# Kernel optimization log

Hardware: AMD Instinct MI355X
Metric: run time of the kernel (lower is better)

The kernel has to match this reference:

```python
import jax, jax.numpy as jnp
import numpy as np

N = 50000      # nodes
E = 1000000    # edges per edge set
D_IN = 2000
D_H = 20
EPS = 1e-5     # BatchNorm eps
SLOPE = 0.01   # leaky_relu negative slope


def setup_inputs() -> dict:
    key = jax.random.key(0)
    ks = jax.random.split(key, 32)
    w = lambda i, shape: jax.random.normal(ks[i], shape, jnp.float32) * 0.05
    inp = {}
    inp["features"] = jax.random.normal(ks[0], (N, D_IN), jnp.float32)
    inp["same_index"] = jax.random.randint(ks[1], (2, 16), 0, N, jnp.int32)
    inp["diff_index"] = jax.random.randint(ks[2], (2, 16), 0, N, jnp.int32)
    inp["edge_index"] = jax.random.randint(ks[3], (2, E), 0, N, jnp.int32)
    inp["same_index2"] = jax.random.randint(ks[4], (2, E), 0, N, jnp.int32)
    inp["diff_index2"] = jax.random.randint(ks[5], (2, E), 0, N, jnp.int32)
    # TransformerConv weights packed as [q,k,v,skip] along axis 0
    inp["c1_W0"] = w(6, (4, D_IN, D_H)); inp["c1_b0"] = w(7, (4, D_H))
    inp["c2_W0"] = w(8, (4, D_IN, D_H)); inp["c2_b0"] = w(9, (4, D_H))
    inp["c1_W"] = w(10, (4, 4, 2 * D_H, D_H)); inp["c1_b"] = w(11, (4, 4, D_H))
    inp["c2_W"] = w(12, (4, 4, 2 * D_H, D_H)); inp["c2_b"] = w(13, (4, 4, D_H))
    inp["c3_W"] = w(14, (5, 4, 2 * D_H, D_H)); inp["c3_b"] = w(15, (5, 4, D_H))  # conv13..17
    inp["bn1_g"] = jnp.ones((5, D_H), jnp.float32); inp["bn1_b"] = w(16, (5, D_H))
    inp["bn2_g"] = jnp.ones((5, D_H), jnp.float32); inp["bn2_b"] = w(17, (5, D_H))
    inp["bn3_g"] = jnp.ones((5, D_H), jnp.float32); inp["bn3_b"] = w(18, (5, D_H))
    inp["fc_W"] = w(19, (5 * D_H, 2)); inp["fc_b"] = w(20, (2,))
    return inp


def _tconv(x, ei, W, b):
    """PyG TransformerConv, heads=1, root_weight=True, concat=True.
    W: [4, Din, 20] = (Wq, Wk, Wv, Wskip); b: [4, 20]."""
    src, dst = ei[0], ei[1]
    q = x @ W[0] + b[0]          # [N,20]
    k = x @ W[1] + b[1]
    v = x @ W[2] + b[2]
    logits = jnp.sum(q[dst] * k[src], axis=-1) / jnp.sqrt(jnp.float32(D_H))  # [E]
    m = jax.ops.segment_max(logits, dst, num_segments=N)
    m = jnp.where(jnp.isfinite(m), m, 0.0)
    e = jnp.exp(logits - m[dst])
    denom = jax.ops.segment_sum(e, dst, num_segments=N)
    alpha = e / jnp.maximum(denom[dst], 1e-16)
    agg = jax.ops.segment_sum(alpha[:, None] * v[src], dst, num_segments=N)  # [N,20]
    return agg + x @ W[3] + b[3]


def _bn(x, g, b):
    mu = jnp.mean(x, axis=0)
    var = jnp.mean(jnp.square(x - mu), axis=0)
    return g * (x - mu) * jax.lax.rsqrt(var + EPS) + b


def _lrelu(x):
    return jnp.where(x >= 0, x, SLOPE * x)


def reference(features, same_index, diff_index, edge_index, same_index2, diff_index2,
              c1_W0, c1_b0, c2_W0, c2_b0, c1_W, c1_b, c2_W, c2_b, c3_W, c3_b,
              bn1_g, bn1_b, bn2_g, bn2_b, bn3_g, bn3_b, fc_W, fc_b):
    # dropout is identity (eval mode)
    x = features
    x1 = _lrelu(_bn(_tconv(x, same_index2, c1_W0, c1_b0), bn1_g[0], bn1_b[0]))
    x2 = _lrelu(_bn(_tconv(x, diff_index2, c2_W0, c2_b0), bn2_g[0], bn2_b[0]))
    h = jnp.concatenate([x1, x2], axis=-1)
    h = _lrelu(_bn(_tconv(h, edge_index, c3_W[0], c3_b[0]), bn3_g[0], bn3_b[0]))
    fc = h
    for l in range(4):
        x3 = jnp.concatenate([x1, x2], axis=-1)
        x4 = jnp.concatenate([x2, x1], axis=-1)
        x1 = _lrelu(_bn(_tconv(x3, same_index2, c1_W[l], c1_b[l]), bn1_g[l + 1], bn1_b[l + 1]))
        x2 = _lrelu(_bn(_tconv(x4, diff_index2, c2_W[l], c2_b[l]), bn2_g[l + 1], bn2_b[l + 1]))
        h = jnp.concatenate([x1, x2], axis=-1)
        h = _lrelu(_bn(_tconv(h, edge_index, c3_W[l + 1], c3_b[l + 1]), bn3_g[l + 1], bn3_b[l + 1]))
        fc = jnp.concatenate([fc, h], axis=-1)
    return fc @ fc_W + fc_b  # [N, 2]
```

## Files before the change

kernel.cpp:

```cpp
#include <hip/hip_runtime.h>
#include <stddef.h>

#define NN 50000
#define NE 1000000
#define SLOT 64
#define RSQRT20 0.22360679774997896f

typedef __attribute__((ext_vector_type(8))) short s16x8;
typedef __attribute__((ext_vector_type(4))) float f32x4;

__device__ __forceinline__ unsigned short f2bf(float x) {
  union { float f; unsigned int u; } cv; cv.f = x;
  unsigned int u = cv.u + 0x7fffu + ((cv.u >> 16) & 1u);
  return (unsigned short)(u >> 16);
}
__device__ __forceinline__ float bf2f(unsigned short h) {
  union { unsigned int u; float f; } cv; cv.u = ((unsigned int)h) << 16;
  return cv.f;
}

__global__ __launch_bounds__(256) void k_zero(int* __restrict__ p, int n) {
  int i = blockIdx.x * 256 + threadIdx.x;
  if (i < n) p[i] = 0;
}

__global__ __launch_bounds__(256) void k_fill(
    const int* __restrict__ s0, const int* __restrict__ d0,
    const int* __restrict__ s1, const int* __restrict__ d1,
    const int* __restrict__ s2, const int* __restrict__ d2,
    int* __restrict__ c0, int* __restrict__ c1, int* __restrict__ c2,
    int* __restrict__ r0, int* __restrict__ r1, int* __restrict__ r2) {
  int e = blockIdx.x * 256 + threadIdx.x;
  if (e >= NE) return;
  const int* s; const int* d; int* c; int* r;
  if (blockIdx.y == 0)      { s = s0; d = d0; c = c0; r = r0; }
  else if (blockIdx.y == 1) { s = s1; d = d1; c = c1; r = r1; }
  else                      { s = s2; d = d2; c = c2; r = r2; }
  int dn = d[e];
  int pos = atomicAdd(&c[dn], 1);
  if (pos < SLOT) r[dn * SLOT + pos] = s[e];
}

__global__ __launch_bounds__(256) void k_packB(
    const float* __restrict__ W1, const float* __restrict__ W2,
    unsigned short* __restrict__ BtH, unsigned short* __restrict__ BtL) {
  int gid = blockIdx.x * 256 + threadIdx.x;
  if (gid >= 160 * 2000) return;
  int col = gid / 2000, k = gid - col * 2000;
  int s = col >= 80; int cc = col - s * 80; int jm = cc / 20, f = cc - jm * 20;
  const float* Wp = s ? W2 : W1;
  float w = Wp[(jm * 2000 + k) * 20 + f];
  unsigned short h = f2bf(w);
  BtH[(size_t)col * 2000 + k] = h;
  BtL[(size_t)col * 2000 + k] = f2bf(w - bf2f(h));
}

__global__ __launch_bounds__(256) void k_mm0(
    const float* __restrict__ X,
    const unsigned short* __restrict__ BtHg, const unsigned short* __restrict__ BtLg,
    const float* __restrict__ B1, const float* __restrict__ B2,
    float* __restrict__ proj, float* __restrict__ stats) {
  __shared__ __attribute__((aligned(16))) char AsH[64 * 128];
  __shared__ __attribute__((aligned(16))) char AsL[64 * 128];
  __shared__ __attribute__((aligned(16))) char BsH[160 * 128];
  __shared__ __attribute__((aligned(16))) char BsL[160 * 128];
  int tid = threadIdx.x;
  if (blockIdx.x == 0 && tid < 120) stats[tid] = 0.f;
  int rowbase = blockIdx.x * 64;
  int l = tid & 63, w = tid >> 6;
  int l15 = l & 15, lq = l >> 4;

  f32x4 acc[10];
  #pragma unroll
  for (int n = 0; n < 10; ++n) acc[n] = (f32x4){0.f, 0.f, 0.f, 0.f};

  float4 aReg[4]; float4 bRegH[5]; float4 bRegL[5];
  auto issue = [&](int tt) {
    int kt = tt * 64;
    #pragma unroll
    for (int i = 0; i < 4; ++i) {
      int idx = tid + i * 256;
      int rowL = idx >> 4, q4 = idx & 15;
      int gr = rowbase + rowL;
      int kk = kt + q4 * 4;
      float4 v = make_float4(0.f, 0.f, 0.f, 0.f);
      if (gr < NN && kk + 4 <= 2000)
        v = *(const float4*)(X + (size_t)gr * 2000 + kk);
      aReg[i] = v;
    }
    #pragma unroll
    for (int i = 0; i < 5; ++i) {
      int idx = tid + i * 256;
      int col = idx >> 3, ck = idx & 7;
      int kk = kt + ck * 8;
      float4 vh = make_float4(0.f, 0.f, 0.f, 0.f);
      float4 vl = vh;
      if (kk + 8 <= 2000) {
        vh = *(const float4*)((const float*)(BtHg + (size_t)col * 2000 + kk));
        vl = *(const float4*)((const float*)(BtLg + (size_t)col * 2000 + kk));
      }
      bRegH[i] = vh; bRegL[i] = vl;
    }
  };

  issue(0);
  for (int t = 0; t < 32; ++t) {
    __syncthreads();
    #pragma unroll
    for (int i = 0; i < 4; ++i) {
      int idx = tid + i * 256;
      int rowL = idx >> 4, q4 = idx & 15;
      ushort4 hh, hl;
      {
        float v0 = aReg[i].x, v1 = aReg[i].y, v2 = aReg[i].z, v3 = aReg[i].w;
        hh.x = f2bf(v0); hl.x = f2bf(v0 - bf2f(hh.x));
        hh.y = f2bf(v1); hl.y = f2bf(v1 - bf2f(hh.y));
        hh.z = f2bf(v2); hl.z = f2bf(v2 - bf2f(hh.z));
        hh.w = f2bf(v3); hl.w = f2bf(v3 - bf2f(hh.w));
      }
      unsigned int byte = (unsigned)rowL * 128u +
          (((unsigned)(q4 * 8)) ^ ((unsigned)((rowL & 7) << 4)));
      *(ushort4*)(AsH + byte) = hh;
      *(ushort4*)(AsL + byte) = hl;
    }
    #pragma unroll
    for (int i = 0; i < 5; ++i) {
      int idx = tid + i * 256;
      int col = idx >> 3, ck = idx & 7;
      unsigned int byte = (unsigned)col * 128u +
          (((unsigned)(ck * 16)) ^ ((unsigned)((col & 7) << 4)));
      *(float4*)(BsH + byte) = bRegH[i];
      *(float4*)(BsL + byte) = bRegL[i];
    }
    __syncthreads();
    if (t < 31) issue(t + 1);
    #pragma unroll
    for (int ks = 0; ks < 2; ++ks) {
      unsigned int rowL = (unsigned)(w * 16 + l15);
      unsigned int ab = rowL * 128u +
          (((unsigned)(ks * 64 + 16 * lq)) ^ ((rowL & 7u) << 4));
      s16x8 afh = *(const s16x8*)(AsH + ab);
      s16x8 afl = *(const s16x8*)(AsL + ab);
      #pragma unroll
      for (int n = 0; n < 10; ++n) {
        unsigned int colL = (unsigned)(n * 16 + l15);
        unsigned int bb = colL * 128u +
            (((unsigned)(ks * 64 + 16 * lq)) ^ ((colL & 7u) << 4));
        s16x8 bfh = *(const s16x8*)(BsH + bb);
        s16x8 bfl = *(const s16x8*)(BsL + bb);
        acc[n] = __builtin_amdgcn_mfma_f32_16x16x32_bf16(afh, bfh, acc[n], 0, 0, 0);
        acc[n] = __builtin_amdgcn_mfma_f32_16x16x32_bf16(afh, bfl, acc[n], 0, 0, 0);
        acc[n] = __builtin_amdgcn_mfma_f32_16x16x32_bf16(afl, bfh, acc[n], 0, 0, 0);
      }
    }
  }

  #pragma unroll
  for (int n = 0; n < 10; ++n) {
    int col = n * 16 + l15;
    int sb = col / 20, f = col - sb * 20;
    float bias = (col < 80) ? B1[col] : B2[col - 80];
    float* ob = proj + (size_t)sb * 1000000;
    #pragma unroll
    for (int r = 0; r < 4; ++r) {
      int row = rowbase + w * 16 + 4 * lq + r;
      if (row < NN) ob[(size_t)row * 20 + f] = acc[n][r] + bias;
    }
  }
}

#define WSTR 812
__global__ __launch_bounds__(256) void k_proj(
    const float* __restrict__ x1, const float* __restrict__ x2,
    const float* __restrict__ W0, const float* __restrict__ B0, int mode0, int slot0,
    const float* __restrict__ W1, const float* __restrict__ B1, int mode1, int slot1,
    const float* __restrict__ W2, const float* __restrict__ B2, int mode2, int slot2,
    int nconv, float* __restrict__ proj, float* __restrict__ stats) {
  __shared__ float wl[12 * WSTR];
  int tid = threadIdx.x;
  if (blockIdx.x == 0 && tid < 120) stats[tid] = 0.f;
  for (int idx = tid; idx < nconv * 3200; idx += 256) {
    int cm = idx / 800, r = idx - cm * 800;
    int t = cm >> 2;
    const float* Wp = (t == 0) ? W0 : (t == 1 ? W1 : W2);
    wl[cm * WSTR + r] = Wp[(cm & 3) * 800 + r];
  }
  __syncthreads();
  int g = tid / 12, cm = tid - g * 12, t = cm >> 2, jm = cm & 3;
  if (g >= 21 || t >= nconv) return;
  int n0 = blockIdx.x * 84 + g * 4;
  if (n0 >= NN) return;
  const float* Bp = (t == 0) ? B0 : (t == 1 ? B1 : B2);
  int mode = (t == 0) ? mode0 : (t == 1 ? mode1 : mode2);
  int slot = (t == 0) ? slot0 : (t == 1 ? slot1 : slot2);
  const float* A  = mode ? x2 : x1;
  const float* Bx = mode ? x1 : x2;
  int nvalid = min(4, NN - n0);
  float4 acc[4][5];
  #pragma unroll
  for (int m = 0; m < 4; ++m)
    #pragma unroll
    for (int f4 = 0; f4 < 5; ++f4)
      acc[m][f4] = make_float4(Bp[jm*20 + f4*4], Bp[jm*20 + f4*4+1],
                               Bp[jm*20 + f4*4+2], Bp[jm*20 + f4*4+3]);
  const float* wbase = &wl[cm * WSTR];
  #pragma unroll 1
  for (int half = 0; half < 2; ++half) {
    const float* src = half ? Bx : A;
    for (int i = 0; i < 20; ++i) {
      float xv[4];
      #pragma unroll
      for (int m = 0; m < 4; ++m)
        xv[m] = (m < nvalid) ? src[(size_t)(n0 + m) * 20 + i] : 0.f;
      #pragma unroll
      for (int f4 = 0; f4 < 5; ++f4) {
        float4 w = *(const float4*)&wbase[(half * 20 + i) * 20 + f4 * 4];
        #pragma unroll
        for (int m = 0; m < 4; ++m) {
          acc[m][f4].x += xv[m] * w.x; acc[m][f4].y += xv[m] * w.y;
          acc[m][f4].z += xv[m] * w.z; acc[m][f4].w += xv[m] * w.w;
        }
      }
    }
  }
  float* ob = proj + (size_t)(slot + jm) * 1000000;
  #pragma unroll
  for (int m = 0; m < 4; ++m) {
    if (m < nvalid) {
      float* p = ob + (size_t)(n0 + m) * 20;
      #pragma unroll
      for (int f4 = 0; f4 < 5; ++f4) *(float4*)&p[f4*4] = acc[m][f4];
    }
  }
}

__global__ __launch_bounds__(256) void k_edge_w(
    const int* __restrict__ cnt, const int* __restrict__ csr,
    const float* __restrict__ q, const float* __restrict__ k,
    float* __restrict__ wsl) {
  int gid = blockIdx.x * 256 + threadIdx.x;
  if (gid >= NN * SLOT) return;
  int n = gid >> 6, j = gid & 63;
  int deg = min(cnt[n], SLOT);
  if (j >= deg) return;
  int s = csr[gid];
  const float* qr = q + (size_t)n * 20;
  const float* kr = k + (size_t)s * 20;
  float dot = 0.f;
  #pragma unroll
  for (int f4 = 0; f4 < 5; ++f4) {
    float4 a = *(const float4*)&qr[f4*4];
    float4 b = *(const float4*)&kr[f4*4];
    dot += a.x*b.x + a.y*b.y + a.z*b.z + a.w*b.w;
  }
  wsl[gid] = __expf(dot * RSQRT20);
}

__global__ __launch_bounds__(256) void k_edge_agg(
    const int* __restrict__ cnt, const int* __restrict__ csr,
    const float* __restrict__ wsl, const float* __restrict__ v,
    const float* __restrict__ skip, float* __restrict__ pre) {
  int gid = blockIdx.x * 256 + threadIdx.x;
  if (gid >= NN * 20) return;
  int n = gid / 20, f = gid - n * 20;
  int deg = min(cnt[n], SLOT);
  const int* cs = csr + n * SLOT;
  const float* ws = wsl + n * SLOT;
  float accd = 0.f, acca = 0.f;
  for (int j = 0; j < deg; ++j) {
    float w = ws[j];
    int s = cs[j];
    acca += w * v[(size_t)s * 20 + f];
    accd += w;
  }
  pre[gid] = acca / fmaxf(accd, 1e-16f) + skip[gid];
}

__global__ __launch_bounds__(320) void k_bnstats(
    const float* __restrict__ p0, const float* __restrict__ p1,
    const float* __restrict__ p2, float* __restrict__ stats) {
  const float* p = (blockIdx.y == 0) ? p0 : (blockIdx.y == 1 ? p1 : p2);
  __shared__ float ls[40];
  int tid = threadIdx.x;
  if (tid < 40) ls[tid] = 0.f;
  __syncthreads();
  int f = tid % 20;
  int c = blockIdx.x * 16 + tid / 20;
  float s = 0.f, sq = 0.f;
  for (int r = c; r < NN; r += 1024) {
    float v = p[r * 20 + f];
    s += v; sq += v * v;
  }
  atomicAdd(&ls[f], s);
  atomicAdd(&ls[20 + f], sq);
  __syncthreads();
  if (tid < 40) atomicAdd(&stats[blockIdx.y * 40 + tid], ls[tid]);
}

__global__ __launch_bounds__(256) void k_bnapply(int nconv,
    const float* __restrict__ pA, const float* __restrict__ gA, const float* __restrict__ bA,
    float* __restrict__ dA, int stA, int ofA,
    const float* __restrict__ pB, const float* __restrict__ gB, const float* __restrict__ bB,
    float* __restrict__ dB, int stB, int ofB,
    const float* __restrict__ pC, const float* __restrict__ gC, const float* __restrict__ bC,
    float* __restrict__ dC, int stC, int ofC,
    const float* __restrict__ stats) {
  int gid = blockIdx.x * 256 + threadIdx.x;
  if (gid >= NN * 20) return;
  int n = gid / 20, f = gid - n * 20;
  for (int c = 0; c < nconv; ++c) {
    const float* p = (c == 0) ? pA : (c == 1 ? pB : pC);
    const float* g = (c == 0) ? gA : (c == 1 ? gB : gC);
    const float* b = (c == 0) ? bA : (c == 1 ? bB : bC);
    float* d = (c == 0) ? dA : (c == 1 ? dB : dC);
    int st = (c == 0) ? stA : (c == 1 ? stB : stC);
    int of = (c == 0) ? ofA : (c == 1 ? ofB : ofC);
    float s1 = stats[c * 40 + f], s2 = stats[c * 40 + 20 + f];
    float mean = s1 * (1.0f / NN);
    float var  = fmaf(-mean, mean, s2 * (1.0f / NN));
    float inv  = rsqrtf(var + 1e-5f);
    float val  = (p[gid] - mean) * inv * g[f] + b[f];
    val = (val >= 0.f) ? val : 0.01f * val;
    d[(size_t)n * st + of + f] = val;
  }
}

__global__ __launch_bounds__(256) void k_fc(
    const float* __restrict__ fc, const float* __restrict__ W,
    const float* __restrict__ b, float* __restrict__ out) {
  int n = blockIdx.x * 256 + threadIdx.x;
  if (n >= NN) return;
  const float* row = fc + (size_t)n * 100;
  float a0 = b[0], a1 = b[1];
  for (int j = 0; j < 100; ++j) {
    float x = row[j];
    a0 += x * W[j * 2];
    a1 += x * W[j * 2 + 1];
  }
  out[n * 2]     = a0;
  out[n * 2 + 1] = a1;
}

extern "C" void kernel_launch(void* const* d_in, const int* in_sizes, int n_in,
                              void* d_out, int out_size, void* d_ws, size_t ws_size,
                              hipStream_t stream) {
  (void)in_sizes; (void)n_in; (void)out_size; (void)ws_size;
  const float* features = (const float*)d_in[0];
  const int* edge_index = (const int*)d_in[3];
  const int* same2      = (const int*)d_in[4];
  const int* diff2      = (const int*)d_in[5];
  const float* c1_W0 = (const float*)d_in[6];
  const float* c1_b0 = (const float*)d_in[7];
  const float* c2_W0 = (const float*)d_in[8];
  const float* c2_b0 = (const float*)d_in[9];
  const float* c1_W  = (const float*)d_in[10];
  const float* c1_b  = (const float*)d_in[11];
  const float* c2_W  = (const float*)d_in[12];
  const float* c2_b  = (const float*)d_in[13];
  const float* c3_W  = (const float*)d_in[14];
  const float* c3_b  = (const float*)d_in[15];
  const float* bn1_g = (const float*)d_in[16];
  const float* bn1_b = (const float*)d_in[17];
  const float* bn2_g = (const float*)d_in[18];
  const float* bn2_b = (const float*)d_in[19];
  const float* bn3_g = (const float*)d_in[20];
  const float* bn3_b = (const float*)d_in[21];
  const float* fc_W  = (const float*)d_in[22];
  const float* fc_b  = (const float*)d_in[23];
  float* out = (float*)d_out;

  char* wsb = (char*)d_ws;
  size_t off = 0;
  auto alloc = [&](size_t bytes) -> void* {
    void* p = wsb + off;
    off += (bytes + 255) & ~(size_t)255;
    return p;
  };
  int*   cntall = (int*)  alloc((size_t)3 * NN * 4);
  int*   csrall = (int*)  alloc((size_t)3 * NN * SLOT * 4);
  float* wslall = (float*)alloc((size_t)3 * NN * SLOT * 4);
  float* proj   = (float*)alloc((size_t)12 * 1000000 * 4);
  float* preA   = (float*)alloc((size_t)1000000 * 4);
  float* preB   = (float*)alloc((size_t)1000000 * 4);
  float* preC   = (float*)alloc((size_t)1000000 * 4);
  float* x1     = (float*)alloc((size_t)1000000 * 4);
  float* x2     = (float*)alloc((size_t)1000000 * 4);
  float* fcbuf  = (float*)alloc((size_t)5000000 * 4);
  float* stats  = (float*)alloc(120 * 4);
  int* cnt0 = cntall;           int* cnt1 = cntall + NN;      int* cnt2 = cntall + 2 * NN;
  int* csr0 = csrall;           int* csr1 = csrall + NN*SLOT; int* csr2 = csrall + 2*NN*SLOT;
  float* wsl0 = wslall;         float* wsl1 = wslall + NN*SLOT; float* wsl2 = wslall + 2*NN*SLOT;
  unsigned short* BtH = (unsigned short*)(proj + (size_t)8 * 1000000);
  unsigned short* BtL = BtH + (size_t)160 * 2000;

  const dim3 B256(256);
  const int gE   = (NE + 255) / 256;
  const int gNF  = (NN * 20 + 255) / 256;
  const int gSL  = (NN * SLOT) / 256;
  const int gMM  = (NN + 63) / 64;
  const int gPR  = (NN + 83) / 84;
  const int gFC  = (NN + 255) / 256;

  k_zero<<<dim3((3 * NN + 255) / 256), B256, 0, stream>>>(cntall, 3 * NN);
  k_fill<<<dim3(gE, 3), B256, 0, stream>>>(
      same2, same2 + NE, diff2, diff2 + NE, edge_index, edge_index + NE,
      cnt0, cnt1, cnt2, csr0, csr1, csr2);

  k_packB<<<dim3((160 * 2000 + 255) / 256), B256, 0, stream>>>(c1_W0, c2_W0, BtH, BtL);
  k_mm0<<<dim3(gMM), B256, 0, stream>>>(features, BtH, BtL, c1_b0, c2_b0, proj, stats);
  k_edge_w<<<dim3(gSL), B256, 0, stream>>>(cnt0, csr0, proj + 0ull,       proj + 1000000ull, wsl0);
  k_edge_w<<<dim3(gSL), B256, 0, stream>>>(cnt1, csr1, proj + 4000000ull, proj + 5000000ull, wsl1);
  k_edge_agg<<<dim3(gNF), B256, 0, stream>>>(cnt0, csr0, wsl0, proj + 2000000ull, proj + 3000000ull, preA);
  k_edge_agg<<<dim3(gNF), B256, 0, stream>>>(cnt1, csr1, wsl1, proj + 6000000ull, proj + 7000000ull, preB);
  k_bnstats<<<dim3(64, 2), dim3(320), 0, stream>>>(preA, preB, preB, stats);
  k_bnapply<<<dim3(gNF), B256, 0, stream>>>(2,
      preA, bn1_g, bn1_b, x1, 20, 0,
      preB, bn2_g, bn2_b, x2, 20, 0,
      preB, bn2_g, bn2_b, x2, 20, 0, stats);

  for (int i = 0; i < 4; ++i) {
    k_proj<<<dim3(gPR), B256, 0, stream>>>(x1, x2,
        c1_W + (size_t)i * 3200, c1_b + (size_t)i * 80, 0, 0,
        c2_W + (size_t)i * 3200, c2_b + (size_t)i * 80, 1, 4,
        c3_W + (size_t)i * 3200, c3_b + (size_t)i * 80, 0, 8,
        3, proj, stats);
    k_edge_w<<<dim3(gSL), B256, 0, stream>>>(cnt0, csr0, proj + 0ull,       proj + 1000000ull, wsl0);
    k_edge_w<<<dim3(gSL), B256, 0, stream>>>(cnt1, csr1, proj + 4000000ull, proj + 5000000ull, wsl1);
    k_edge_w<<<dim3(gSL), B256, 0, stream>>>(cnt2, csr2, proj + 8000000ull, proj + 9000000ull, wsl2);
    k_edge_agg<<<dim3(gNF), B256, 0, stream>>>(cnt0, csr0, wsl0, proj + 2000000ull,  proj + 3000000ull,  preA);
    k_edge_agg<<<dim3(gNF), B256, 0, stream>>>(cnt1, csr1, wsl1, proj + 6000000ull,  proj + 7000000ull,  preB);
    k_edge_agg<<<dim3(gNF), B256, 0, stream>>>(cnt2, csr2, wsl2, proj + 10000000ull, proj + 11000000ull, preC);
    k_bnstats<<<dim3(64, 3), dim3(320), 0, stream>>>(preA, preB, preC, stats);
    k_bnapply<<<dim3(gNF), B256, 0, stream>>>(3,
        preA, bn1_g + (i + 1) * 20, bn1_b + (i + 1) * 20, x1, 20, 0,
        preB, bn2_g + (i + 1) * 20, bn2_b + (i + 1) * 20, x2, 20, 0,
        preC, bn3_g + i * 20,       bn3_b + i * 20,       fcbuf, 100, i * 20, stats);
  }

  k_proj<<<dim3(gPR), B256, 0, stream>>>(x1, x2,
      c3_W + 4 * 3200, c3_b + 4 * 80, 0, 8,
      c3_W + 4 * 3200, c3_b + 4 * 80, 0, 0,
      c3_W + 4 * 3200, c3_b + 4 * 80, 0, 0,
      1, proj, stats);
  k_edge_w<<<dim3(gSL), B256, 0, stream>>>(cnt2, csr2, proj + 8000000ull, proj + 9000000ull, wsl2);
  k_edge_agg<<<dim3(gNF), B256, 0, stream>>>(cnt2, csr2, wsl2, proj + 10000000ull, proj + 11000000ull, preC);
  k_bnstats<<<dim3(64, 1), dim3(320), 0, stream>>>(preC, preC, preC, stats);
  k_bnapply<<<dim3(gNF), B256, 0, stream>>>(1,
      preC, bn3_g + 80, bn3_b + 80, fcbuf, 100, 80,
      preC, bn3_g + 80, bn3_b + 80, fcbuf, 100, 80,
      preC, bn3_g + 80, bn3_b + 80, fcbuf, 100, 80, stats);

  k_fc<<<dim3(gFC), B256, 0, stream>>>(fcbuf, fc_W, fc_b, out);
}
```

Baseline: 2.105 ms.

## Fuse edge attention weight and aggregation kernels, store CSR indices as u16

The separate per-edge weight kernel and per-feature aggregation kernel are merged into one kernel. Each 64-lane wavefront handles one node: it computes the edge softmax numerators into shared memory, reduces the denominator with shuffles, and aggregates V across 3 lane groups of 20 features. This removes the intermediate weight buffer's global write and read, and halves the launch count. CSR source indices are also stored as 16-bit values to cut index traffic. That is valid only because node ids stay below 65536, and the code relies on wavefront-synchronous shared-memory access with no barrier.

```diff
diff --git a/kernel.cpp b/kernel.cpp
--- a/kernel.cpp
+++ b/kernel.cpp
@@ -29,16 +29,17 @@
     const int* __restrict__ s1, const int* __restrict__ d1,
     const int* __restrict__ s2, const int* __restrict__ d2,
     int* __restrict__ c0, int* __restrict__ c1, int* __restrict__ c2,
-    int* __restrict__ r0, int* __restrict__ r1, int* __restrict__ r2) {
+    unsigned short* __restrict__ r0, unsigned short* __restrict__ r1,
+    unsigned short* __restrict__ r2) {
   int e = blockIdx.x * 256 + threadIdx.x;
   if (e >= NE) return;
-  const int* s; const int* d; int* c; int* r;
+  const int* s; const int* d; int* c; unsigned short* r;
   if (blockIdx.y == 0)      { s = s0; d = d0; c = c0; r = r0; }
   else if (blockIdx.y == 1) { s = s1; d = d1; c = c1; r = r1; }
   else                      { s = s2; d = d2; c = c2; r = r2; }
   int dn = d[e];
   int pos = atomicAdd(&c[dn], 1);
-  if (pos < SLOT) r[dn * SLOT + pos] = s[e];
+  if (pos < SLOT) r[dn * SLOT + pos] = (unsigned short)s[e];
 }
 
 __global__ __launch_bounds__(256) void k_packB(
@@ -234,46 +235,52 @@
   }
 }
 
-__global__ __launch_bounds__(256) void k_edge_w(
-    const int* __restrict__ cnt, const int* __restrict__ csr,
+__global__ __launch_bounds__(256) void k_edge_fused(
+    const int* __restrict__ cnt, const unsigned short* __restrict__ csr,
     const float* __restrict__ q, const float* __restrict__ k,
-    float* __restrict__ wsl) {
-  int gid = blockIdx.x * 256 + threadIdx.x;
-  if (gid >= NN * SLOT) return;
-  int n = gid >> 6, j = gid & 63;
+    const float* __restrict__ v, const float* __restrict__ skip,
+    float* __restrict__ pre) {
+  __shared__ float lw[4][64];
+  __shared__ unsigned short lsrc[4][64];
+  int tid = threadIdx.x;
+  int wv = tid >> 6, j = tid & 63;
+  int n = blockIdx.x * 4 + wv;
+  if (n >= NN) return;
   int deg = min(cnt[n], SLOT);
-  if (j >= deg) return;
-  int s = csr[gid];
-  const float* qr = q + (size_t)n * 20;
-  const float* kr = k + (size_t)s * 20;
-  float dot = 0.f;
+  float w = 0.f; int s = 0;
+  if (j < deg) {
+    s = csr[n * SLOT + j];
+    const float* qr = q + (size_t)n * 20;
+    const float* kr = k + (size_t)s * 20;
+    float dot = 0.f;
+    #pragma unroll
+    for (int f4 = 0; f4 < 5; ++f4) {
+      float4 a = *(const float4*)&qr[f4*4];
+      float4 b = *(const float4*)&kr[f4*4];
+      dot += a.x*b.x + a.y*b.y + a.z*b.z + a.w*b.w;
+    }
+    w = __expf(dot * RSQRT20);
+  }
+  lw[wv][j] = w;
+  lsrc[wv][j] = (unsigned short)s;
+  float accd = w;
   #pragma unroll
-  for (int f4 = 0; f4 < 5; ++f4) {
-    float4 a = *(const float4*)&qr[f4*4];
-    float4 b = *(const float4*)&kr[f4*4];
-    dot += a.x*b.x + a.y*b.y + a.z*b.z + a.w*b.w;
-  }
-  wsl[gid] = __expf(dot * RSQRT20);
-}
-
-__global__ __launch_bounds__(256) void k_edge_agg(
-    const int* __restrict__ cnt, const int* __restrict__ csr,
-    const float* __restrict__ wsl, const float* __restrict__ v,
-    const float* __restrict__ skip, float* __restrict__ pre) {
-  int gid = blockIdx.x * 256 + threadIdx.x;
-  if (gid >= NN * 20) return;
-  int n = gid / 20, f = gid - n * 20;
-  int deg = min(cnt[n], SLOT);
-  const int* cs = csr + n * SLOT;
-  const float* ws = wsl + n * SLOT;
-  float accd = 0.f, acca = 0.f;
-  for (int j = 0; j < deg; ++j) {
-    float w = ws[j];
-    int s = cs[j];
-    acca += w * v[(size_t)s * 20 + f];
-    accd += w;
-  }
-  pre[gid] = acca / fmaxf(accd, 1e-16f) + skip[gid];
+  for (int off = 1; off < 64; off <<= 1) accd += __shfl_xor(accd, off);
+  int f = j % 20, jg = j / 20;
+  float acca = 0.f;
+  if (j < 60) {
+    for (int jj = jg; jj < deg; jj += 3) {
+      float wj = lw[wv][jj];
+      int sj = lsrc[wv][jj];
+      acca += wj * v[(size_t)sj * 20 + f];
+    }
+  }
+  float g1 = __shfl(acca, f + 20);
+  float g2 = __shfl(acca, f + 40);
+  if (j < 20) {
+    float val = (acca + g1 + g2) / fmaxf(accd, 1e-16f) + skip[(size_t)n * 20 + j];
+    pre[(size_t)n * 20 + j] = val;
+  }
 }
 
 __global__ __launch_bounds__(320) void k_bnstats(
@@ -376,9 +383,8 @@
     off += (bytes + 255) & ~(size_t)255;
     return p;
   };
-  int*   cntall = (int*)  alloc((size_t)3 * NN * 4);
-  int*   csrall = (int*)  alloc((size_t)3 * NN * SLOT * 4);
-  float* wslall = (float*)alloc((size_t)3 * NN * SLOT * 4);
+  int*            cntall = (int*)           alloc((size_t)3 * NN * 4);
+  unsigned short* csrall = (unsigned short*)alloc((size_t)3 * NN * SLOT * 2);
   float* proj   = (float*)alloc((size_t)12 * 1000000 * 4);
   float* preA   = (float*)alloc((size_t)1000000 * 4);
   float* preB   = (float*)alloc((size_t)1000000 * 4);
@@ -387,16 +393,17 @@
   float* x2     = (float*)alloc((size_t)1000000 * 4);
   float* fcbuf  = (float*)alloc((size_t)5000000 * 4);
   float* stats  = (float*)alloc(120 * 4);
-  int* cnt0 = cntall;           int* cnt1 = cntall + NN;      int* cnt2 = cntall + 2 * NN;
-  int* csr0 = csrall;           int* csr1 = csrall + NN*SLOT; int* csr2 = csrall + 2*NN*SLOT;
-  float* wsl0 = wslall;         float* wsl1 = wslall + NN*SLOT; float* wsl2 = wslall + 2*NN*SLOT;
+  int* cnt0 = cntall;  int* cnt1 = cntall + NN;  int* cnt2 = cntall + 2 * NN;
+  unsigned short* csr0 = csrall;
+  unsigned short* csr1 = csrall + (size_t)NN * SLOT;
+  unsigned short* csr2 = csrall + (size_t)2 * NN * SLOT;
   unsigned short* BtH = (unsigned short*)(proj + (size_t)8 * 1000000);
   unsigned short* BtL = BtH + (size_t)160 * 2000;
 
   const dim3 B256(256);
   const int gE   = (NE + 255) / 256;
   const int gNF  = (NN * 20 + 255) / 256;
-  const int gSL  = (NN * SLOT) / 256;
+  const int gEF  = (NN + 3) / 4;
   const int gMM  = (NN + 63) / 64;
   const int gPR  = (NN + 83) / 84;
   const int gFC  = (NN + 255) / 256;
@@ -408,10 +415,10 @@
 
   k_packB<<<dim3((160 * 2000 + 255) / 256), B256, 0, stream>>>(c1_W0, c2_W0, BtH, BtL);
   k_mm0<<<dim3(gMM), B256, 0, stream>>>(features, BtH, BtL, c1_b0, c2_b0, proj, stats);
-  k_edge_w<<<dim3(gSL), B256, 0, stream>>>(cnt0, csr0, proj + 0ull,       proj + 1000000ull, wsl0);
-  k_edge_w<<<dim3(gSL), B256, 0, stream>>>(cnt1, csr1, proj + 4000000ull, proj + 5000000ull, wsl1);
-  k_edge_agg<<<dim3(gNF), B256, 0, stream>>>(cnt0, csr0, wsl0, proj + 2000000ull, proj + 3000000ull, preA);
-  k_edge_agg<<<dim3(gNF), B256, 0, stream>>>(cnt1, csr1, wsl1, proj + 6000000ull, proj + 7000000ull, preB);
+  k_edge_fused<<<dim3(gEF), B256, 0, stream>>>(cnt0, csr0,
+      proj + 0ull, proj + 1000000ull, proj + 2000000ull, proj + 3000000ull, preA);
+  k_edge_fused<<<dim3(gEF), B256, 0, stream>>>(cnt1, csr1,
+      proj + 4000000ull, proj + 5000000ull, proj + 6000000ull, proj + 7000000ull, preB);
   k_bnstats<<<dim3(64, 2), dim3(320), 0, stream>>>(preA, preB, preB, stats);
   k_bnapply<<<dim3(gNF), B256, 0, stream>>>(2,
       preA, bn1_g, bn1_b, x1, 20, 0,
@@ -424,12 +431,12 @@
         c2_W + (size_t)i * 3200, c2_b + (size_t)i * 80, 1, 4,
         c3_W + (size_t)i * 3200, c3_b + (size_t)i * 80, 0, 8,
         3, proj, stats);
-    k_edge_w<<<dim3(gSL), B256, 0, stream>>>(cnt0, csr0, proj + 0ull,       proj + 1000000ull, wsl0);
-    k_edge_w<<<dim3(gSL), B256, 0, stream>>>(cnt1, csr1, proj + 4000000ull, proj + 5000000ull, wsl1);
-    k_edge_w<<<dim3(gSL), B256, 0, stream>>>(cnt2, csr2, proj + 8000000ull, proj + 9000000ull, wsl2);
-    k_edge_agg<<<dim3(gNF), B256, 0, stream>>>(cnt0, csr0, wsl0, proj + 2000000ull,  proj + 3000000ull,  preA);
-    k_edge_agg<<<dim3(gNF), B256, 0, stream>>>(cnt1, csr1, wsl1, proj + 6000000ull,  proj + 7000000ull,  preB);
-    k_edge_agg<<<dim3(gNF), B256, 0, stream>>>(cnt2, csr2, wsl2, proj + 10000000ull, proj + 11000000ull, preC);
+    k_edge_fused<<<dim3(gEF), B256, 0, stream>>>(cnt0, csr0,
+        proj + 0ull, proj + 1000000ull, proj + 2000000ull, proj + 3000000ull, preA);
+    k_edge_fused<<<dim3(gEF), B256, 0, stream>>>(cnt1, csr1,
+        proj + 4000000ull, proj + 5000000ull, proj + 6000000ull, proj + 7000000ull, preB);
+    k_edge_fused<<<dim3(gEF), B256, 0, stream>>>(cnt2, csr2,
+        proj + 8000000ull, proj + 9000000ull, proj + 10000000ull, proj + 11000000ull, preC);
     k_bnstats<<<dim3(64, 3), dim3(320), 0, stream>>>(preA, preB, preC, stats);
     k_bnapply<<<dim3(gNF), B256, 0, stream>>>(3,
         preA, bn1_g + (i + 1) * 20, bn1_b + (i + 1) * 20, x1, 20, 0,
@@ -442,8 +449,8 @@
       c3_W + 4 * 3200, c3_b + 4 * 80, 0, 0,
       c3_W + 4 * 3200, c3_b + 4 * 80, 0, 0,
       1, proj, stats);
-  k_edge_w<<<dim3(gSL), B256, 0, stream>>>(cnt2, csr2, proj + 8000000ull, proj + 9000000ull, wsl2);
-  k_edge_agg<<<dim3(gNF), B256, 0, stream>>>(cnt2, csr2, wsl2, proj + 10000000ull, proj + 11000000ull, preC);
+  k_edge_fused<<<dim3(gEF), B256, 0, stream>>>(cnt2, csr2,
+      proj + 8000000ull, proj + 9000000ull, proj + 10000000ull, proj + 11000000ull, preC);
   k_bnstats<<<dim3(64, 1), dim3(320), 0, stream>>>(preC, preC, preC, stats);
   k_bnapply<<<dim3(gNF), B256, 0, stream>>>(1,
       preC, bn3_g + 80, bn3_b + 80, fcbuf, 100, 80,
```

New measurement: 1.853 ms. 12.0% less time.
